# Optimization experiments

Measured on AMD Instinct MI355X. Metric: run time of the kernel, lower is better.

Reference implementation:

```python
import jax, jax.numpy as jnp
import numpy as np


def setup_inputs() -> dict:
    key = jax.random.key(0)
    ks = jax.random.split(key, 5)
    B, C, hl, wl = 8, 256, 64, 64
    hh, wh = 32, 32
    qd = 64
    return {
        "low_level": jax.random.normal(ks[0], (B, C, hl, wl), dtype=jnp.float32),
        "high_level": jax.random.normal(ks[1], (B, C, hh, wh), dtype=jnp.float32),
        "Wq": jax.random.normal(ks[2], (qd, C), dtype=jnp.float32) * 0.02,
        "bq": jnp.zeros((qd,), dtype=jnp.float32),
        "Wk": jax.random.normal(ks[3], (qd, C), dtype=jnp.float32) * 0.02,
        "bk": jnp.zeros((qd,), dtype=jnp.float32),
        "gamma": jnp.zeros((1,), dtype=jnp.float32),
    }


def reference(low_level, high_level, Wq, bq, Wk, bk, gamma):
    B, C, hl, wl = low_level.shape
    _, _, hh, wh = high_level.shape
    Nl, Nh = hl * wl, hh * wh
    # 1x1 conv projections (conv1x1 == channel matmul)
    # query: [B, Nl, qd]
    q = jnp.einsum("bchw,qc->bhwq", low_level, Wq).reshape(B, Nl, -1) + bq
    # key: [B, qd, Nh]
    k = jnp.einsum("bchw,qc->bqhw", high_level, Wk).reshape(B, -1, Nh) + bk[None, :, None]
    # energy [B, Nl, Nh], softmax over key positions (last dim), no scaling
    energy = jnp.einsum("blq,bqh->blh", q, k)
    attention = jax.nn.softmax(energy, axis=-1)
    # value = raw high_level features; out[b,c,l] = sum_h value[b,c,h] * attention[b,l,h]
    value = high_level.reshape(B, C, Nh)
    out = jnp.einsum("bch,blh->bcl", value, attention).reshape(B, C, hl, wl)
    return gamma[0] * out + low_level
```

## Files before the change

kernel.cpp:

```cpp
#include <hip/hip_runtime.h>
#include <stdint.h>


#define APAD 40

typedef __attribute__((ext_vector_type(8))) short bf16x8;
typedef __attribute__((ext_vector_type(4))) float f32x4;

typedef const __attribute__((address_space(1))) uint32_t* gp1_t;
typedef __attribute__((address_space(3))) uint32_t* sp3_t;

__device__ __forceinline__ uint32_t f2bf(float f) {
    uint32_t u = __builtin_bit_cast(uint32_t, f);
    return (u + 0x7FFFu + ((u >> 16) & 1u)) >> 16;
}
__device__ __forceinline__ bf16x8 asbf(uint4 v) { return __builtin_bit_cast(bf16x8, v); }

__device__ __forceinline__ void async16(void* lds, const void* g) {
    __builtin_amdgcn_global_load_lds((gp1_t)g, (sp3_t)lds, 16, 0, 0);
}

union U8 { uint16_t u[8]; bf16x8 v; };
__device__ __forceinline__ bf16x8 pack8(const float* f) {
    U8 t;
#pragma unroll
    for (int i = 0; i < 8; ++i) t.u[i] = (uint16_t)f2bf(f[i]);
    return t.v;
}

__global__ __launch_bounds__(256) void prep(
    const float* __restrict__ low, const float* __restrict__ high,
    const float* __restrict__ Wq, const float* __restrict__ bq,
    const float* __restrict__ Wk, const float* __restrict__ bk,
    uint16_t* __restrict__ qws, uint16_t* __restrict__ kws,
    uint16_t* __restrict__ vws)
{
    __shared__ uint16_t Alds[64 * APAD];
    int bid = blockIdx.x, tid = threadIdx.x;

    if (bid >= 640) {
        int v = bid - 640;
#pragma unroll
        for (int it = 0; it < 4; ++it) {
            int t = it * 65536 + v * 256 + tid;
            int row = t >> 7, seg = t & 127;
            int b = row >> 8, c = row & 255;
            int h0 = seg << 3;
            const float* src = high + ((size_t)row << 10) + h0;
            float4 a = *(const float4*)src;
            float4 d = *(const float4*)(src + 4);
            uint4 val;
            val.x = f2bf(a.x) | (f2bf(a.y) << 16);
            val.y = f2bf(a.z) | (f2bf(a.w) << 16);
            val.z = f2bf(d.x) | (f2bf(d.y) << 16);
            val.w = f2bf(d.z) | (f2bf(d.w) << 16);
            int ck = h0 >> 5, hl = h0 & 31;
            *(uint4*)((char*)vws +
                ((size_t)((b * 32 + ck) * 256 + c)) * 64 +
                (size_t)((hl * 2) ^ ((c & 3) << 4))) = val;
        }
        return;
    }

    const float* X; const float* W; const float* bias;
    int xstride, isq, drow0;
    if (bid < 512) {
        int b = bid >> 6, lt = bid & 63;
        X = low + ((size_t)b << 20) + lt * 64;  xstride = 4096;
        W = Wq; bias = bq; isq = 1; drow0 = b * 4096 + lt * 64;
    } else {
        int r = bid - 512; int b = r >> 4, hb = r & 15;
        X = high + ((size_t)b << 18) + hb * 64; xstride = 1024;
        W = Wk; bias = bk; isq = 0; drow0 = b * 1024 + hb * 64;
    }
    int w = tid >> 6, lane = tid & 63, g = lane >> 4, lcol = lane & 15;
    int p = tid >> 4, lg = tid & 15;
    int qd = w * 16 + lcol;
    f32x4 acc[4];
#pragma unroll
    for (int i = 0; i < 4; ++i) acc[i] = (f32x4){0.f, 0.f, 0.f, 0.f};

#pragma unroll 1
    for (int cs = 0; cs < 8; ++cs) {
        int c0 = cs * 32;
        const float* r0 = X + (size_t)(c0 + p * 2) * xstride + lg * 4;
        float4 x0 = *(const float4*)r0;
        float4 x1 = *(const float4*)(r0 + xstride);
        const float* wr = W + qd * 256 + c0 + g * 8;
        float4 wa = *(const float4*)wr;
        float4 wb = *(const float4*)(wr + 4);
        __syncthreads();
        const float* px0 = (const float*)&x0;
        const float* px1 = (const float*)&x1;
#pragma unroll
        for (int j = 0; j < 4; ++j)
            *(uint32_t*)&Alds[(lg * 4 + j) * APAD + p * 2] =
                f2bf(px0[j]) | (f2bf(px1[j]) << 16);
        __syncthreads();
        float wf[8] = {wa.x, wa.y, wa.z, wa.w, wb.x, wb.y, wb.z, wb.w};
        bf16x8 bfrag = pack8(wf);
#pragma unroll
        for (int mt = 0; mt < 4; ++mt) {
            bf16x8 af = *(const bf16x8*)&Alds[(mt * 16 + lcol) * APAD + g * 8];
            acc[mt] = __builtin_amdgcn_mfma_f32_16x16x32_bf16(af, bfrag, acc[mt], 0, 0, 0);
        }
    }
    float bv = bias[qd];
    if (isq) {
#pragma unroll
        for (int mt = 0; mt < 4; ++mt)
#pragma unroll
            for (int r = 0; r < 4; ++r)
                qws[(size_t)(drow0 + mt * 16 + g * 4 + r) * 64 + qd] =
                    (uint16_t)f2bf(acc[mt][r] + bv);
    } else {
#pragma unroll
        for (int mt = 0; mt < 4; ++mt)
#pragma unroll
            for (int r = 0; r < 4; ++r) {
                int hl = mt * 16 + g * 4 + r;
                *(uint16_t*)((char*)kws + (size_t)(drow0 + hl) * 128 +
                    (size_t)((qd * 2) ^ ((hl & 7) << 4))) =
                    (uint16_t)f2bf(acc[mt][r] + bv);
            }
    }
}

__global__ __launch_bounds__(256, 3) void attn(
    const float* __restrict__ low, const float* __restrict__ gamma_p,
    const uint16_t* __restrict__ qws, const uint16_t* __restrict__ kws,
    const uint16_t* __restrict__ vws, float* __restrict__ out)
{
    __shared__ char smem[43264];
    char* Vc = smem;
    char* Kc = smem + 32768;
    char* Pl = smem + 40960;
    float* rs = (float*)(smem + 43008);

    int bid = blockIdx.x;
    int blk = (bid & 7) * 128 + (bid >> 3);
    int b = blk >> 7;
    int l0 = (blk & 127) * 32;
    int tid = threadIdx.x, w = tid >> 6, lane = tid & 63;
    int g = lane >> 4, lcol = lane & 15;
    int wtl = w >> 1, wth = w & 1;

    const char* Qb = (const char*)qws + ((size_t)(b * 4096 + l0)) * 128;
    const char* Kb = (const char*)kws + ((size_t)b * 1024) * 128;
    const char* Vb = (const char*)vws + (size_t)b * 524288;

#define STAGE(ck, buf)                                                        \
    {                                                                         \
        const char* vg_ = Vb + (ck) * 16384;                                  \
        const char* kg_ = Kb + (ck) * 4096;                                   \
        char* vl_ = Vc + (buf) * 16384;                                       \
        char* kl_ = Kc + (buf) * 4096;                                        \
        _Pragma("unroll")                                                     \
        for (int r_ = 0; r_ < 5; ++r_) {                                      \
            int s_ = r_ * 4 + w;                                              \
            if (s_ < 16) async16(vl_ + s_ * 1024, vg_ + s_ * 1024 + lane * 16);\
            else async16(kl_ + (s_ - 16) * 1024, kg_ + (s_ - 16) * 1024 + lane * 16);\
        }                                                                     \
    }

    STAGE(0, 0);

    bf16x8 qf[2];
#pragma unroll
    for (int ks = 0; ks < 2; ++ks)
        qf[ks] = asbf(*(const uint4*)(Qb + (wtl * 16 + lcol) * 128 + ks * 64 + g * 16));

    f32x4 oacc[2][4];
#pragma unroll
    for (int i = 0; i < 2; ++i)
#pragma unroll
        for (int j = 0; j < 4; ++j) oacc[i][j] = (f32x4){0.f, 0.f, 0.f, 0.f};
    float rowp[4] = {0.f, 0.f, 0.f, 0.f};

    int hK = wth * 16 + lcol;

#pragma unroll 1
    for (int ck = 0; ck < 32; ++ck) {
        int buf = ck & 1;
        if (ck + 1 < 32) {
            STAGE(ck + 1, buf ^ 1);
            asm volatile("s_waitcnt vmcnt(5)" ::: "memory");
        } else {
            asm volatile("s_waitcnt vmcnt(0)" ::: "memory");
        }
        __builtin_amdgcn_sched_barrier(0);
        __builtin_amdgcn_s_barrier();

        const char* kl = Kc + buf * 4096;
        f32x4 sacc = (f32x4){0.f, 0.f, 0.f, 0.f};
#pragma unroll
        for (int ks = 0; ks < 2; ++ks) {
            bf16x8 kf = *(const bf16x8*)(kl + hK * 128 +
                          (((ks * 64 + g * 16) ^ ((hK & 7) << 4))));
            sacc = __builtin_amdgcn_mfma_f32_16x16x32_bf16(qf[ks], kf, sacc, 0, 0, 0);
        }
#pragma unroll
        for (int r = 0; r < 4; ++r) {
            int l = wtl * 16 + g * 4 + r;
            float pv = __expf(sacc[r]);
            rowp[r] += pv;
            *(uint16_t*)(Pl + l * 64 + (((wth * 16 + lcol) * 2) ^ ((l & 3) << 4))) =
                (uint16_t)f2bf(pv);
        }
        asm volatile("s_waitcnt lgkmcnt(0)" ::: "memory");
        __builtin_amdgcn_sched_barrier(0);
        __builtin_amdgcn_s_barrier();

        const char* vl = Vc + buf * 16384;
        bf16x8 pf[2];
#pragma unroll
        for (int mt = 0; mt < 2; ++mt) {
            int l = mt * 16 + lcol;
            pf[mt] = *(const bf16x8*)(Pl + l * 64 + ((g * 16) ^ ((l & 3) << 4)));
        }
#pragma unroll
        for (int ct = 0; ct < 4; ++ct) {
            int c = w * 64 + ct * 16 + lcol;
            bf16x8 vf = *(const bf16x8*)(vl + c * 64 + ((g * 16) ^ ((c & 3) << 4)));
#pragma unroll
            for (int mt = 0; mt < 2; ++mt)
                oacc[mt][ct] = __builtin_amdgcn_mfma_f32_16x16x32_bf16(pf[mt], vf, oacc[mt][ct], 0, 0, 0);
        }
        __builtin_amdgcn_sched_barrier(0);
        __builtin_amdgcn_s_barrier();
    }

#pragma unroll
    for (int r = 0; r < 4; ++r) {
        float v = rowp[r];
        v += __shfl_xor(v, 1, 64);
        v += __shfl_xor(v, 2, 64);
        v += __shfl_xor(v, 4, 64);
        v += __shfl_xor(v, 8, 64);
        rowp[r] = v;
    }
    if (lcol == 0) {
#pragma unroll
        for (int r = 0; r < 4; ++r) rs[w * 16 + g * 4 + r] = rowp[r];
    }
    __syncthreads();

    float gam = gamma_p[0];
    float inv[2][4];
#pragma unroll
    for (int mt = 0; mt < 2; ++mt)
#pragma unroll
        for (int r = 0; r < 4; ++r) {
            int li = g * 4 + r;
            inv[mt][r] = gam / (rs[mt * 32 + li] + rs[mt * 32 + 16 + li]);
        }

#pragma unroll
    for (int mt = 0; mt < 2; ++mt)
#pragma unroll
        for (int ct = 0; ct < 4; ++ct) {
            int c = w * 64 + ct * 16 + lcol;
            size_t base = ((size_t)(b * 256 + c) << 12) + l0 + mt * 16 + g * 4;
            float4 lo = *(const float4*)(low + base);
            float4 res;
            res.x = lo.x + oacc[mt][ct][0] * inv[mt][0];
            res.y = lo.y + oacc[mt][ct][1] * inv[mt][1];
            res.z = lo.z + oacc[mt][ct][2] * inv[mt][2];
            res.w = lo.w + oacc[mt][ct][3] * inv[mt][3];
            *(float4*)(out + base) = res;
        }
}

extern "C" void kernel_launch(void* const* d_in, const int* in_sizes, int n_in,
                              void* d_out, int out_size, void* d_ws, size_t ws_size,
                              hipStream_t stream) {
    const float* low   = (const float*)d_in[0];
    const float* high  = (const float*)d_in[1];
    const float* Wq    = (const float*)d_in[2];
    const float* bq    = (const float*)d_in[3];
    const float* Wk    = (const float*)d_in[4];
    const float* bk    = (const float*)d_in[5];
    const float* gamma = (const float*)d_in[6];
    float* out = (float*)d_out;

    uint16_t* qws = (uint16_t*)d_ws;
    uint16_t* kws = (uint16_t*)((char*)d_ws + (4u << 20));
    uint16_t* vws = (uint16_t*)((char*)d_ws + (5u << 20));

    prep<<<dim3(896), dim3(256), 0, stream>>>(low, high, Wq, bq, Wk, bk, qws, kws, vws);
    attn<<<dim3(1024), dim3(256), 0, stream>>>(low, gamma, qws, kws, vws, out);
}
```

Measured before the change: 160.0 us.

## Fuse Q projection into attention kernel and pass P via shuffles

Moves the query 1x1-conv projection out of the prep kernel and into the attention kernel, so the bf16 Q workspace is no longer written and re-read. Restructures the attention loop so each wave computes transposed scores and rebuilds the P fragment with lane shuffles instead of an LDS round trip, which removes one barrier per chunk. It also double-buffers the prep LDS tile to drop a barrier and raises launch bounds to 4 blocks per CU. The trade-offs are extra redundant low-level reads and Wq reads per attention block, plus scalar output stores in place of float4 stores.

```diff
diff --git a/kernel.cpp b/kernel.cpp
--- a/kernel.cpp
+++ b/kernel.cpp
@@ -14,8 +14,9 @@
     uint32_t u = __builtin_bit_cast(uint32_t, f);
     return (u + 0x7FFFu + ((u >> 16) & 1u)) >> 16;
 }
-__device__ __forceinline__ bf16x8 asbf(uint4 v) { return __builtin_bit_cast(bf16x8, v); }
-
+__device__ __forceinline__ uint32_t pk2(float a, float b) {
+    return f2bf(a) | (f2bf(b) << 16);
+}
 __device__ __forceinline__ void async16(void* lds, const void* g) {
     __builtin_amdgcn_global_load_lds((gp1_t)g, (sp3_t)lds, 16, 0, 0);
 }
@@ -28,114 +29,93 @@
     return t.v;
 }
 
-__global__ __launch_bounds__(256) void prep(
-    const float* __restrict__ low, const float* __restrict__ high,
-    const float* __restrict__ Wq, const float* __restrict__ bq,
+__global__ __launch_bounds__(256) void kvprep(
+    const float* __restrict__ high,
     const float* __restrict__ Wk, const float* __restrict__ bk,
-    uint16_t* __restrict__ qws, uint16_t* __restrict__ kws,
-    uint16_t* __restrict__ vws)
+    uint16_t* __restrict__ kws, uint16_t* __restrict__ vws)
 {
-    __shared__ uint16_t Alds[64 * APAD];
+    __shared__ uint16_t Alds[2 * 64 * APAD];
     int bid = blockIdx.x, tid = threadIdx.x;
 
-    if (bid >= 640) {
-        int v = bid - 640;
+    if (bid >= 128) {
+        int v = bid - 128;
 #pragma unroll
         for (int it = 0; it < 4; ++it) {
             int t = it * 65536 + v * 256 + tid;
             int row = t >> 7, seg = t & 127;
-            int b = row >> 8, c = row & 255;
+            int vb = row >> 8, c = row & 255;
             int h0 = seg << 3;
             const float* src = high + ((size_t)row << 10) + h0;
             float4 a = *(const float4*)src;
             float4 d = *(const float4*)(src + 4);
             uint4 val;
-            val.x = f2bf(a.x) | (f2bf(a.y) << 16);
-            val.y = f2bf(a.z) | (f2bf(a.w) << 16);
-            val.z = f2bf(d.x) | (f2bf(d.y) << 16);
-            val.w = f2bf(d.z) | (f2bf(d.w) << 16);
+            val.x = pk2(a.x, a.y);
+            val.y = pk2(a.z, a.w);
+            val.z = pk2(d.x, d.y);
+            val.w = pk2(d.z, d.w);
             int ck = h0 >> 5, hl = h0 & 31;
             *(uint4*)((char*)vws +
-                ((size_t)((b * 32 + ck) * 256 + c)) * 64 +
+                ((size_t)((vb * 32 + ck) * 256 + c)) * 64 +
                 (size_t)((hl * 2) ^ ((c & 3) << 4))) = val;
         }
         return;
     }
 
-    const float* X; const float* W; const float* bias;
-    int xstride, isq, drow0;
-    if (bid < 512) {
-        int b = bid >> 6, lt = bid & 63;
-        X = low + ((size_t)b << 20) + lt * 64;  xstride = 4096;
-        W = Wq; bias = bq; isq = 1; drow0 = b * 4096 + lt * 64;
-    } else {
-        int r = bid - 512; int b = r >> 4, hb = r & 15;
-        X = high + ((size_t)b << 18) + hb * 64; xstride = 1024;
-        W = Wk; bias = bk; isq = 0; drow0 = b * 1024 + hb * 64;
-    }
+    int kb = bid >> 4, hb = bid & 15;
+    const float* X = high + ((size_t)kb << 18) + hb * 64;
     int w = tid >> 6, lane = tid & 63, g = lane >> 4, lcol = lane & 15;
     int p = tid >> 4, lg = tid & 15;
     int qd = w * 16 + lcol;
     f32x4 acc[4];
 #pragma unroll
     for (int i = 0; i < 4; ++i) acc[i] = (f32x4){0.f, 0.f, 0.f, 0.f};
-
 #pragma unroll 1
     for (int cs = 0; cs < 8; ++cs) {
         int c0 = cs * 32;
-        const float* r0 = X + (size_t)(c0 + p * 2) * xstride + lg * 4;
+        uint16_t* Ab = Alds + (cs & 1) * (64 * APAD);
+        const float* r0 = X + (size_t)(c0 + p * 2) * 1024 + lg * 4;
         float4 x0 = *(const float4*)r0;
-        float4 x1 = *(const float4*)(r0 + xstride);
-        const float* wr = W + qd * 256 + c0 + g * 8;
+        float4 x1 = *(const float4*)(r0 + 1024);
+        const float* wr = Wk + qd * 256 + c0 + g * 8;
         float4 wa = *(const float4*)wr;
         float4 wb = *(const float4*)(wr + 4);
-        __syncthreads();
         const float* px0 = (const float*)&x0;
         const float* px1 = (const float*)&x1;
 #pragma unroll
         for (int j = 0; j < 4; ++j)
-            *(uint32_t*)&Alds[(lg * 4 + j) * APAD + p * 2] =
-                f2bf(px0[j]) | (f2bf(px1[j]) << 16);
+            *(uint32_t*)&Ab[(lg * 4 + j) * APAD + p * 2] = pk2(px0[j], px1[j]);
         __syncthreads();
         float wf[8] = {wa.x, wa.y, wa.z, wa.w, wb.x, wb.y, wb.z, wb.w};
         bf16x8 bfrag = pack8(wf);
 #pragma unroll
         for (int mt = 0; mt < 4; ++mt) {
-            bf16x8 af = *(const bf16x8*)&Alds[(mt * 16 + lcol) * APAD + g * 8];
+            bf16x8 af = *(const bf16x8*)&Ab[(mt * 16 + lcol) * APAD + g * 8];
             acc[mt] = __builtin_amdgcn_mfma_f32_16x16x32_bf16(af, bfrag, acc[mt], 0, 0, 0);
         }
     }
-    float bv = bias[qd];
-    if (isq) {
-#pragma unroll
-        for (int mt = 0; mt < 4; ++mt)
-#pragma unroll
-            for (int r = 0; r < 4; ++r)
-                qws[(size_t)(drow0 + mt * 16 + g * 4 + r) * 64 + qd] =
-                    (uint16_t)f2bf(acc[mt][r] + bv);
-    } else {
-#pragma unroll
-        for (int mt = 0; mt < 4; ++mt)
-#pragma unroll
-            for (int r = 0; r < 4; ++r) {
-                int hl = mt * 16 + g * 4 + r;
-                *(uint16_t*)((char*)kws + (size_t)(drow0 + hl) * 128 +
-                    (size_t)((qd * 2) ^ ((hl & 7) << 4))) =
-                    (uint16_t)f2bf(acc[mt][r] + bv);
-            }
-    }
-}
-
-__global__ __launch_bounds__(256, 3) void attn(
-    const float* __restrict__ low, const float* __restrict__ gamma_p,
-    const uint16_t* __restrict__ qws, const uint16_t* __restrict__ kws,
-    const uint16_t* __restrict__ vws, float* __restrict__ out)
+    float bkv = bk[qd];
+    char* kdst = (char*)kws + (size_t)(kb * 1024 + hb * 64) * 128;
+#pragma unroll
+    for (int mt = 0; mt < 4; ++mt)
+#pragma unroll
+        for (int r = 0; r < 4; ++r) {
+            int hl = mt * 16 + g * 4 + r;
+            *(uint16_t*)(kdst + hl * 128 + (((qd * 2) ^ ((hl & 7) << 4)))) =
+                (uint16_t)f2bf(acc[mt][r] + bkv);
+        }
+}
+
+__global__ __launch_bounds__(256, 4) void attn(
+    const float* __restrict__ low, const float* __restrict__ Wq,
+    const float* __restrict__ bq, const float* __restrict__ gamma_p,
+    const uint16_t* __restrict__ kws, const uint16_t* __restrict__ vws,
+    float* __restrict__ out)
 {
-    __shared__ char smem[43264];
+    __shared__ char smem[40960];
     char* Vc = smem;
     char* Kc = smem + 32768;
-    char* Pl = smem + 40960;
-    float* rs = (float*)(smem + 43008);
+    uint16_t* Alds = (uint16_t*)smem;
+    char* Qlds = smem + 8192;
 
     int bid = blockIdx.x;
     int blk = (bid & 7) * 128 + (bid >> 3);
@@ -143,18 +123,75 @@
     int l0 = (blk & 127) * 32;
     int tid = threadIdx.x, w = tid >> 6, lane = tid & 63;
     int g = lane >> 4, lcol = lane & 15;
-    int wtl = w >> 1, wth = w & 1;
-
-    const char* Qb = (const char*)qws + ((size_t)(b * 4096 + l0)) * 128;
-    const char* Kb = (const char*)kws + ((size_t)b * 1024) * 128;
+    int wl = w & 1, wc = w >> 1;
+
+    const float* lowb = low + ((size_t)b << 20);
+    int qd = w * 16 + lcol;
+
+    f32x4 qacc[2];
+    qacc[0] = (f32x4){0.f, 0.f, 0.f, 0.f};
+    qacc[1] = (f32x4){0.f, 0.f, 0.f, 0.f};
+    {
+        int cpair = tid >> 3, lseg = tid & 7;
+#pragma unroll 1
+        for (int cs = 0; cs < 8; ++cs) {
+            int c0 = cs * 32;
+            uint16_t* Ab = Alds + (cs & 1) * (32 * APAD);
+            if (tid < 128) {
+                const float* r0 = lowb + (size_t)(c0 + cpair * 2) * 4096 + l0 + lseg * 4;
+                float4 x0 = *(const float4*)r0;
+                float4 x1 = *(const float4*)(r0 + 4096);
+                const float* px0 = (const float*)&x0;
+                const float* px1 = (const float*)&x1;
+#pragma unroll
+                for (int j = 0; j < 4; ++j)
+                    *(uint32_t*)&Ab[(lseg * 4 + j) * APAD + cpair * 2] =
+                        pk2(px0[j], px1[j]);
+            }
+            const float* wr = Wq + qd * 256 + c0 + g * 8;
+            float4 wa = *(const float4*)wr;
+            float4 wb = *(const float4*)(wr + 4);
+            __syncthreads();
+            float wf[8] = {wa.x, wa.y, wa.z, wa.w, wb.x, wb.y, wb.z, wb.w};
+            bf16x8 bfrag = pack8(wf);
+#pragma unroll
+            for (int mt = 0; mt < 2; ++mt) {
+                bf16x8 af = *(const bf16x8*)&Ab[(mt * 16 + lcol) * APAD + g * 8];
+                qacc[mt] = __builtin_amdgcn_mfma_f32_16x16x32_bf16(af, bfrag, qacc[mt], 0, 0, 0);
+            }
+        }
+    }
+    {
+        float bqv = bq[qd];
+#pragma unroll
+        for (int mt = 0; mt < 2; ++mt)
+#pragma unroll
+            for (int r = 0; r < 4; ++r) {
+                int l = mt * 16 + g * 4 + r;
+                *(uint16_t*)(Qlds + l * 128 + (((qd * 2) ^ ((l & 7) << 4)))) =
+                    (uint16_t)f2bf(qacc[mt][r] + bqv);
+            }
+    }
+    __syncthreads();
+    bf16x8 qB[2];
+    {
+        int lq = wl * 16 + lcol;
+#pragma unroll
+        for (int kp = 0; kp < 2; ++kp)
+            qB[kp] = *(const bf16x8*)(Qlds + lq * 128 +
+                      (((kp * 64 + g * 16) ^ ((lq & 7) << 4))));
+    }
+    __syncthreads();
+
+    const char* Kb = (const char*)kws + (size_t)b * 131072;
     const char* Vb = (const char*)vws + (size_t)b * 524288;
 
-#define STAGE(ck, buf)                                                        \
+#define STAGE(ck, bf_)                                                        \
     {                                                                         \
         const char* vg_ = Vb + (ck) * 16384;                                  \
         const char* kg_ = Kb + (ck) * 4096;                                   \
-        char* vl_ = Vc + (buf) * 16384;                                       \
-        char* kl_ = Kc + (buf) * 4096;                                        \
+        char* vl_ = Vc + (bf_) * 16384;                                       \
+        char* kl_ = Kc + (bf_) * 4096;                                        \
         _Pragma("unroll")                                                     \
         for (int r_ = 0; r_ < 5; ++r_) {                                      \
             int s_ = r_ * 4 + w;                                              \
@@ -164,111 +201,87 @@
     }
 
     STAGE(0, 0);
-
-    bf16x8 qf[2];
-#pragma unroll
-    for (int ks = 0; ks < 2; ++ks)
-        qf[ks] = asbf(*(const uint4*)(Qb + (wtl * 16 + lcol) * 128 + ks * 64 + g * 16));
-
-    f32x4 oacc[2][4];
-#pragma unroll
-    for (int i = 0; i < 2; ++i)
-#pragma unroll
-        for (int j = 0; j < 4; ++j) oacc[i][j] = (f32x4){0.f, 0.f, 0.f, 0.f};
-    float rowp[4] = {0.f, 0.f, 0.f, 0.f};
-
-    int hK = wth * 16 + lcol;
+    asm volatile("s_waitcnt vmcnt(0)" ::: "memory");
+    __builtin_amdgcn_sched_barrier(0);
+    __builtin_amdgcn_s_barrier();
+
+    f32x4 oacc[8];
+#pragma unroll
+    for (int i = 0; i < 8; ++i) oacc[i] = (f32x4){0.f, 0.f, 0.f, 0.f};
+    float rowp = 0.f;
+    int sl0 = ((g & 1) << 5) + lcol;
+    int sl1 = sl0 + 16;
+    bool hiG = (g >= 2);
 
 #pragma unroll 1
     for (int ck = 0; ck < 32; ++ck) {
         int buf = ck & 1;
+        if (ck + 1 < 32) STAGE(ck + 1, buf ^ 1);
+
+        const char* kl = Kc + buf * 4096;
+        f32x4 sacc0 = (f32x4){0.f, 0.f, 0.f, 0.f};
+        f32x4 sacc1 = (f32x4){0.f, 0.f, 0.f, 0.f};
+#pragma unroll
+        for (int kp = 0; kp < 2; ++kp) {
+            bf16x8 ka0 = *(const bf16x8*)(kl + lcol * 128 +
+                           (((kp * 64 + g * 16) ^ ((lcol & 7) << 4))));
+            sacc0 = __builtin_amdgcn_mfma_f32_16x16x32_bf16(ka0, qB[kp], sacc0, 0, 0, 0);
+            int h1 = 16 + lcol;
+            bf16x8 ka1 = *(const bf16x8*)(kl + h1 * 128 +
+                           (((kp * 64 + g * 16) ^ ((h1 & 7) << 4))));
+            sacc1 = __builtin_amdgcn_mfma_f32_16x16x32_bf16(ka1, qB[kp], sacc1, 0, 0, 0);
+        }
+
+        float e0[4], e1[4];
+#pragma unroll
+        for (int r = 0; r < 4; ++r) { e0[r] = __expf(sacc0[r]); e1[r] = __expf(sacc1[r]); }
+        rowp += (e0[0] + e0[1]) + (e0[2] + e0[3]) + (e1[0] + e1[1]) + (e1[2] + e1[3]);
+        uint32_t pAx = pk2(e0[0], e0[1]), pAy = pk2(e0[2], e0[3]);
+        uint32_t pBx = pk2(e1[0], e1[1]), pBy = pk2(e1[2], e1[3]);
+        uint32_t a0 = (uint32_t)__shfl((int)pAx, sl0, 64);
+        uint32_t a1 = (uint32_t)__shfl((int)pAy, sl0, 64);
+        uint32_t a2 = (uint32_t)__shfl((int)pAx, sl1, 64);
+        uint32_t a3 = (uint32_t)__shfl((int)pAy, sl1, 64);
+        uint32_t b0 = (uint32_t)__shfl((int)pBx, sl0, 64);
+        uint32_t b1 = (uint32_t)__shfl((int)pBy, sl0, 64);
+        uint32_t b2 = (uint32_t)__shfl((int)pBx, sl1, 64);
+        uint32_t b3 = (uint32_t)__shfl((int)pBy, sl1, 64);
+        uint4 pw;
+        pw.x = hiG ? b0 : a0;
+        pw.y = hiG ? b1 : a1;
+        pw.z = hiG ? b2 : a2;
+        pw.w = hiG ? b3 : a3;
+        bf16x8 pfrag = __builtin_bit_cast(bf16x8, pw);
+
+        const char* vl = Vc + buf * 16384;
+#pragma unroll
+        for (int ct = 0; ct < 8; ++ct) {
+            int c = wc * 128 + ct * 16 + lcol;
+            bf16x8 va = *(const bf16x8*)(vl + c * 64 + (((g * 16) ^ ((c & 3) << 4))));
+            oacc[ct] = __builtin_amdgcn_mfma_f32_16x16x32_bf16(va, pfrag, oacc[ct], 0, 0, 0);
+        }
+
         if (ck + 1 < 32) {
-            STAGE(ck + 1, buf ^ 1);
-            asm volatile("s_waitcnt vmcnt(5)" ::: "memory");
-        } else {
             asm volatile("s_waitcnt vmcnt(0)" ::: "memory");
-        }
-        __builtin_amdgcn_sched_barrier(0);
-        __builtin_amdgcn_s_barrier();
-
-        const char* kl = Kc + buf * 4096;
-        f32x4 sacc = (f32x4){0.f, 0.f, 0.f, 0.f};
-#pragma unroll
-        for (int ks = 0; ks < 2; ++ks) {
-            bf16x8 kf = *(const bf16x8*)(kl + hK * 128 +
-                          (((ks * 64 + g * 16) ^ ((hK & 7) << 4))));
-            sacc = __builtin_amdgcn_mfma_f32_16x16x32_bf16(qf[ks], kf, sacc, 0, 0, 0);
-        }
+            __builtin_amdgcn_sched_barrier(0);
+            __builtin_amdgcn_s_barrier();
+        }
+    }
+
+    rowp += __shfl_xor(rowp, 16, 64);
+    rowp += __shfl_xor(rowp, 32, 64);
+    float inv = gamma_p[0] / rowp;
+
+    int l = l0 + wl * 16 + lcol;
+#pragma unroll
+    for (int ct = 0; ct < 8; ++ct) {
 #pragma unroll
         for (int r = 0; r < 4; ++r) {
-            int l = wtl * 16 + g * 4 + r;
-            float pv = __expf(sacc[r]);
-            rowp[r] += pv;
-            *(uint16_t*)(Pl + l * 64 + (((wth * 16 + lcol) * 2) ^ ((l & 3) << 4))) =
-                (uint16_t)f2bf(pv);
-        }
-        asm volatile("s_waitcnt lgkmcnt(0)" ::: "memory");
-        __builtin_amdgcn_sched_barrier(0);
-        __builtin_amdgcn_s_barrier();
-
-        const char* vl = Vc + buf * 16384;
-        bf16x8 pf[2];
-#pragma unroll
-        for (int mt = 0; mt < 2; ++mt) {
-            int l = mt * 16 + lcol;
-            pf[mt] = *(const bf16x8*)(Pl + l * 64 + ((g * 16) ^ ((l & 3) << 4)));
-        }
-#pragma unroll
-        for (int ct = 0; ct < 4; ++ct) {
-            int c = w * 64 + ct * 16 + lcol;
-            bf16x8 vf = *(const bf16x8*)(vl + c * 64 + ((g * 16) ^ ((c & 3) << 4)));
-#pragma unroll
-            for (int mt = 0; mt < 2; ++mt)
-                oacc[mt][ct] = __builtin_amdgcn_mfma_f32_16x16x32_bf16(pf[mt], vf, oacc[mt][ct], 0, 0, 0);
-        }
-        __builtin_amdgcn_sched_barrier(0);
-        __builtin_amdgcn_s_barrier();
-    }
-
-#pragma unroll
-    for (int r = 0; r < 4; ++r) {
-        float v = rowp[r];
-        v += __shfl_xor(v, 1, 64);
-        v += __shfl_xor(v, 2, 64);
-        v += __shfl_xor(v, 4, 64);
-        v += __shfl_xor(v, 8, 64);
-        rowp[r] = v;
-    }
-    if (lcol == 0) {
-#pragma unroll
-        for (int r = 0; r < 4; ++r) rs[w * 16 + g * 4 + r] = rowp[r];
-    }
-    __syncthreads();
-
-    float gam = gamma_p[0];
-    float inv[2][4];
-#pragma unroll
-    for (int mt = 0; mt < 2; ++mt)
-#pragma unroll
-        for (int r = 0; r < 4; ++r) {
-            int li = g * 4 + r;
-            inv[mt][r] = gam / (rs[mt * 32 + li] + rs[mt * 32 + 16 + li]);
-        }
-
-#pragma unroll
-    for (int mt = 0; mt < 2; ++mt)
-#pragma unroll
-        for (int ct = 0; ct < 4; ++ct) {
-            int c = w * 64 + ct * 16 + lcol;
-            size_t base = ((size_t)(b * 256 + c) << 12) + l0 + mt * 16 + g * 4;
-            float4 lo = *(const float4*)(low + base);
-            float4 res;
-            res.x = lo.x + oacc[mt][ct][0] * inv[mt][0];
-            res.y = lo.y + oacc[mt][ct][1] * inv[mt][1];
-            res.z = lo.z + oacc[mt][ct][2] * inv[mt][2];
-            res.w = lo.w + oacc[mt][ct][3] * inv[mt][3];
-            *(float4*)(out + base) = res;
-        }
+            int c = wc * 128 + ct * 16 + g * 4 + r;
+            size_t idx = ((size_t)(b * 256 + c) << 12) + l;
+            out[idx] = low[idx] + oacc[ct][r] * inv;
+        }
+    }
 }
 
 extern "C" void kernel_launch(void* const* d_in, const int* in_sizes, int n_in,
@@ -283,10 +296,9 @@
     const float* gamma = (const float*)d_in[6];
     float* out = (float*)d_out;
 
-    uint16_t* qws = (uint16_t*)d_ws;
-    uint16_t* kws = (uint16_t*)((char*)d_ws + (4u << 20));
-    uint16_t* vws = (uint16_t*)((char*)d_ws + (5u << 20));
-
-    prep<<<dim3(896), dim3(256), 0, stream>>>(low, high, Wq, bq, Wk, bk, qws, kws, vws);
-    attn<<<dim3(1024), dim3(256), 0, stream>>>(low, gamma, qws, kws, vws, out);
-}
+    uint16_t* kws = (uint16_t*)d_ws;
+    uint16_t* vws = (uint16_t*)((char*)d_ws + (1u << 20));
+
+    kvprep<<<dim3(384), dim3(256), 0, stream>>>(high, Wk, bk, kws, vws);
+    attn<<<dim3(1024), dim3(256), 0, stream>>>(low, Wq, bq, gamma, kws, vws, out);
+}
```

New measurement: 160.6 us. Within noise of the previous version (+0.4%).
